# Kernel tuning notes

Measured on AMD Instinct MI355X. Metric: run time of the kernel, lower is better.

## Reference

```python
import jax, jax.numpy as jnp
import numpy as np

B, T, H, M = 64, 1024, 512, 256  # batch, max_time, out_dim(=annot_dim), memory_dim


def setup_inputs() -> dict:
    key = jax.random.key(0)
    ks = jax.random.split(key, 13)
    s = lambda k, shape, scale=1.0: jax.random.normal(k, shape, dtype=jnp.float32) * scale
    return {
        "memory": s(ks[0], (B, M)),
        "context": s(ks[1], (B, H)),
        "rnn_state": s(ks[2], (B, H)),
        "annotations": s(ks[3], (B, T, H)),
        "W_ih": s(ks[4], (3 * H, H + M), 0.04),
        "b_ih": s(ks[5], (3 * H,), 0.04),
        "W_hh": s(ks[6], (3 * H, H), 0.04),
        "b_hh": s(ks[7], (3 * H,), 0.04),
        "Wq": s(ks[8], (H, H), 0.04),
        "bq": s(ks[9], (H,), 0.04),
        "Wa": s(ks[10], (H, H), 0.04),
        "ba": s(ks[11], (H,), 0.04),
        "v": s(ks[12], (H,), 0.04),
    }


def reference(memory, context, rnn_state, annotations,
              W_ih, b_ih, W_hh, b_hh, Wq, bq, Wa, ba, v):
    # --- GRUCell step (torch semantics) ---
    x = jnp.concatenate([memory, context], axis=-1)          # (B, M+H)
    gi = x @ W_ih.T + b_ih                                   # (B, 3H)
    gh = rnn_state @ W_hh.T + b_hh                           # (B, 3H)
    i_r, i_z, i_n = jnp.split(gi, 3, axis=-1)
    h_r, h_z, h_n = jnp.split(gh, 3, axis=-1)
    r = jax.nn.sigmoid(i_r + h_r)
    z = jax.nn.sigmoid(i_z + h_z)
    n = jnp.tanh(i_n + r * h_n)
    h_new = (1.0 - z) * n + z * rnn_state                    # (B, H)

    # --- Bahdanau additive attention ---
    pq = h_new @ Wq.T + bq                                   # (B, H)
    pa = annotations @ Wa.T + ba                             # (B, T, H)
    scores = jnp.tanh(pq[:, None, :] + pa) @ v               # (B, T)
    align = jax.nn.softmax(scores, axis=-1)                  # (B, T)
    ctx = jnp.einsum('bt,btd->bd', align, annotations)       # (B, H)
    return (h_new, ctx, align)
```

## Files before the change

### kernel.cpp

```cpp
#include <hip/hip_runtime.h>
#include <hip/hip_bf16.h>


typedef __attribute__((ext_vector_type(8))) __bf16 bf16x8;
typedef __attribute__((ext_vector_type(8))) unsigned short u16x8;
typedef __attribute__((ext_vector_type(4))) float f32x4;

__device__ __forceinline__ unsigned short f2bf(float f) {
    __hip_bfloat16 h = __float2bfloat16(f);
    return __builtin_bit_cast(unsigned short, h);
}
__device__ __forceinline__ float tanh_fast(float x) {
    float e = __expf(2.0f * x);
    return 1.0f - 2.0f / (e + 1.0f);
}
__device__ __forceinline__ float sigmoid_f(float x) {
    return 1.0f / (1.0f + __expf(-x));
}
__device__ __forceinline__ int swz(int x) { return x ^ (((x >> 8) & 7) << 4); }

__global__ __launch_bounds__(256) void wconv_kernel(
    const float* __restrict__ W_ih, const float* __restrict__ W_hh,
    const float* __restrict__ Wq, const float* __restrict__ Wa,
    unsigned short* __restrict__ WihB, unsigned short* __restrict__ WhhB,
    unsigned short* __restrict__ WqB, unsigned short* __restrict__ WaB)
{
    const int cb = blockIdx.x * 4 + (threadIdx.x >> 6);
    const int l = threadIdx.x & 63;
    const float* src;
    unsigned short* dst;
    int K, local, NB, kt;
    if (cb < 2304) {
        src = W_ih; dst = WihB; K = 768; local = cb;
        NB = local / 24; kt = local % 24;
    } else if (cb < 3840) {
        src = W_hh; dst = WhhB; K = 512; local = cb - 2304;
        NB = local >> 4; kt = local & 15;
    } else if (cb < 4352) {
        src = Wq; dst = WqB; K = 512; local = cb - 3840;
        NB = local >> 4; kt = local & 15;
    } else {
        src = Wa; dst = WaB; K = 512; local = cb - 4352;
        NB = local >> 4; kt = local & 15;
    }
    const float* s = src + (size_t)(NB * 16 + (l & 15)) * K + kt * 32 + (l >> 4) * 8;
    float4 f0 = *(const float4*)s;
    float4 f1 = *(const float4*)(s + 4);
    u16x8 p;
    p[0] = f2bf(f0.x); p[1] = f2bf(f0.y); p[2] = f2bf(f0.z); p[3] = f2bf(f0.w);
    p[4] = f2bf(f1.x); p[5] = f2bf(f1.y); p[6] = f2bf(f1.z); p[7] = f2bf(f1.w);
    *(u16x8*)&dst[(size_t)local * 512 + l * 8] = p;
}

#define CVT8(f0, f1, AF)                                                           \
    {                                                                              \
        u16x8 p_;                                                                  \
        p_[0] = f2bf((f0).x); p_[1] = f2bf((f0).y); p_[2] = f2bf((f0).z); p_[3] = f2bf((f0).w); \
        p_[4] = f2bf((f1).x); p_[5] = f2bf((f1).y); p_[6] = f2bf((f1).z); p_[7] = f2bf((f1).w); \
        AF = __builtin_bit_cast(bf16x8, p_);                                       \
    }

__global__ __launch_bounds__(64) void gru_kernel(
    const float* __restrict__ memory, const float* __restrict__ context,
    const float* __restrict__ rnn_state,
    const unsigned short* __restrict__ WihB, const float* __restrict__ b_ih,
    const unsigned short* __restrict__ WhhB, const float* __restrict__ b_hh,
    float* __restrict__ h_new)
{
    const int l = threadIdx.x;
    const int mt = blockIdx.x >> 5;
    const int hb = blockIdx.x & 31;
    const int r = l & 15, g = l >> 4;
    const int row = mt * 16 + r;

    f32x4 a_ir = {0,0,0,0}, a_iz = {0,0,0,0}, a_in = {0,0,0,0};
    f32x4 a_hr = {0,0,0,0}, a_hz = {0,0,0,0}, a_hn = {0,0,0,0};

#pragma unroll
    for (int kt = 0; kt < 8; ++kt) {
        const float* s = memory + (size_t)row * 256 + kt * 32 + g * 8;
        float4 f0 = *(const float4*)s, f1 = *(const float4*)(s + 4);
        bf16x8 af; CVT8(f0, f1, af);
        bf16x8 b0 = __builtin_bit_cast(bf16x8, *(const u16x8*)&WihB[((size_t)(hb) * 24 + kt) * 512 + l * 8]);
        bf16x8 b1 = __builtin_bit_cast(bf16x8, *(const u16x8*)&WihB[((size_t)(32 + hb) * 24 + kt) * 512 + l * 8]);
        bf16x8 b2 = __builtin_bit_cast(bf16x8, *(const u16x8*)&WihB[((size_t)(64 + hb) * 24 + kt) * 512 + l * 8]);
        a_ir = __builtin_amdgcn_mfma_f32_16x16x32_bf16(af, b0, a_ir, 0, 0, 0);
        a_iz = __builtin_amdgcn_mfma_f32_16x16x32_bf16(af, b1, a_iz, 0, 0, 0);
        a_in = __builtin_amdgcn_mfma_f32_16x16x32_bf16(af, b2, a_in, 0, 0, 0);
    }
#pragma unroll
    for (int kt = 8; kt < 24; ++kt) {
        const float* s = context + (size_t)row * 512 + (kt - 8) * 32 + g * 8;
        float4 f0 = *(const float4*)s, f1 = *(const float4*)(s + 4);
        bf16x8 af; CVT8(f0, f1, af);
        bf16x8 b0 = __builtin_bit_cast(bf16x8, *(const u16x8*)&WihB[((size_t)(hb) * 24 + kt) * 512 + l * 8]);
        bf16x8 b1 = __builtin_bit_cast(bf16x8, *(const u16x8*)&WihB[((size_t)(32 + hb) * 24 + kt) * 512 + l * 8]);
        bf16x8 b2 = __builtin_bit_cast(bf16x8, *(const u16x8*)&WihB[((size_t)(64 + hb) * 24 + kt) * 512 + l * 8]);
        a_ir = __builtin_amdgcn_mfma_f32_16x16x32_bf16(af, b0, a_ir, 0, 0, 0);
        a_iz = __builtin_amdgcn_mfma_f32_16x16x32_bf16(af, b1, a_iz, 0, 0, 0);
        a_in = __builtin_amdgcn_mfma_f32_16x16x32_bf16(af, b2, a_in, 0, 0, 0);
    }
#pragma unroll
    for (int kt = 0; kt < 16; ++kt) {
        const float* s = rnn_state + (size_t)row * 512 + kt * 32 + g * 8;
        float4 f0 = *(const float4*)s, f1 = *(const float4*)(s + 4);
        bf16x8 af; CVT8(f0, f1, af);
        bf16x8 b0 = __builtin_bit_cast(bf16x8, *(const u16x8*)&WhhB[((size_t)(hb) * 16 + kt) * 512 + l * 8]);
        bf16x8 b1 = __builtin_bit_cast(bf16x8, *(const u16x8*)&WhhB[((size_t)(32 + hb) * 16 + kt) * 512 + l * 8]);
        bf16x8 b2 = __builtin_bit_cast(bf16x8, *(const u16x8*)&WhhB[((size_t)(64 + hb) * 16 + kt) * 512 + l * 8]);
        a_hr = __builtin_amdgcn_mfma_f32_16x16x32_bf16(af, b0, a_hr, 0, 0, 0);
        a_hz = __builtin_amdgcn_mfma_f32_16x16x32_bf16(af, b1, a_hz, 0, 0, 0);
        a_hn = __builtin_amdgcn_mfma_f32_16x16x32_bf16(af, b2, a_hn, 0, 0, 0);
    }
    const int c = hb * 16 + r;
    const float bir = b_ih[c], biz = b_ih[512 + c], bin = b_ih[1024 + c];
    const float bhr = b_hh[c], bhz = b_hh[512 + c], bhn = b_hh[1024 + c];
#pragma unroll
    for (int r2 = 0; r2 < 4; ++r2) {
        const int m = mt * 16 + g * 4 + r2;
        float rr = sigmoid_f(a_ir[r2] + bir + a_hr[r2] + bhr);
        float zz = sigmoid_f(a_iz[r2] + biz + a_hz[r2] + bhz);
        float nn = tanh_fast(a_in[r2] + bin + rr * (a_hn[r2] + bhn));
        float h0 = rnn_state[(size_t)m * 512 + c];
        h_new[(size_t)m * 512 + c] = (1.f - zz) * nn + zz * h0;
    }
}

__global__ __launch_bounds__(64) void pq_kernel(
    const float* __restrict__ h_new, const unsigned short* __restrict__ WqB,
    const float* __restrict__ bq, const float* __restrict__ ba,
    float* __restrict__ q)
{
    const int l = threadIdx.x;
    const int mt = blockIdx.x >> 5;
    const int hb = blockIdx.x & 31;
    const int r = l & 15, g = l >> 4;
    const int row = mt * 16 + r;
    f32x4 acc = {0,0,0,0};
#pragma unroll
    for (int kt = 0; kt < 16; ++kt) {
        const float* s = h_new + (size_t)row * 512 + kt * 32 + g * 8;
        float4 f0 = *(const float4*)s, f1 = *(const float4*)(s + 4);
        bf16x8 af; CVT8(f0, f1, af);
        bf16x8 b0 = __builtin_bit_cast(bf16x8, *(const u16x8*)&WqB[((size_t)hb * 16 + kt) * 512 + l * 8]);
        acc = __builtin_amdgcn_mfma_f32_16x16x32_bf16(af, b0, acc, 0, 0, 0);
    }
    const int c = hb * 16 + r;
    const float add = bq[c] + ba[c];
#pragma unroll
    for (int r2 = 0; r2 < 4; ++r2)
        q[(size_t)(mt * 16 + g * 4 + r2) * 512 + c] = acc[r2] + add;
}

__global__ __launch_bounds__(256, 2) void scores_kernel(
    const float* __restrict__ ann, const unsigned short* __restrict__ WaB,
    const float* __restrict__ qv, const float* __restrict__ v,
    float* __restrict__ scores)
{
    __shared__ unsigned short As[32768];
    __shared__ float s_sc[64];
    const int tid = threadIdx.x;
    const int l = tid & 63;
    const int w = tid >> 6;
    const int r0 = blockIdx.x * 64;
    const int b = blockIdx.x >> 4;

    if (tid < 64) s_sc[tid] = 0.f;

#pragma unroll
    for (int p = 0; p < 16; ++p) {
        int cidx = tid + p * 256;
        int row = cidx >> 6;
        int c8 = cidx & 63;
        int kt = c8 >> 2, g = c8 & 3;
        int rt = row >> 4, r15 = row & 15;
        const float* s = ann + (size_t)(r0 + row) * 512 + c8 * 8;
        float4 f0 = *(const float4*)s, f1 = *(const float4*)(s + 4);
        u16x8 pk;
        pk[0] = f2bf(f0.x); pk[1] = f2bf(f0.y); pk[2] = f2bf(f0.z); pk[3] = f2bf(f0.w);
        pk[4] = f2bf(f1.x); pk[5] = f2bf(f1.y); pk[6] = f2bf(f1.z); pk[7] = f2bf(f1.w);
        int logical = (((rt * 16 + kt) * 64) + g * 16 + r15) * 16;
        *(u16x8*)((char*)As + swz(logical)) = pk;
    }
    __syncthreads();

    f32x4 acc[4][8];
#pragma unroll
    for (int i = 0; i < 4; ++i)
#pragma unroll
        for (int j = 0; j < 8; ++j) acc[i][j] = (f32x4){0.f, 0.f, 0.f, 0.f};

#pragma unroll 2
    for (int kt = 0; kt < 16; ++kt) {
        u16x8 bv[8];
#pragma unroll
        for (int ct = 0; ct < 8; ++ct)
            bv[ct] = *(const u16x8*)(WaB + ((size_t)((w * 8 + ct) * 16 + kt)) * 512 + l * 8);
#pragma unroll
        for (int rt = 0; rt < 4; ++rt) {
            int logical = ((rt * 16 + kt) * 64 + l) * 16;
            bf16x8 af = __builtin_bit_cast(bf16x8, *(const u16x8*)((char*)As + swz(logical)));
#pragma unroll
            for (int ct = 0; ct < 8; ++ct)
                acc[rt][ct] = __builtin_amdgcn_mfma_f32_16x16x32_bf16(
                    af, __builtin_bit_cast(bf16x8, bv[ct]), acc[rt][ct], 0, 0, 0);
        }
    }

    float rsum[4][4];
#pragma unroll
    for (int i = 0; i < 4; ++i)
#pragma unroll
        for (int j = 0; j < 4; ++j) rsum[i][j] = 0.f;

#pragma unroll
    for (int ct = 0; ct < 8; ++ct) {
        int col = w * 128 + ct * 16 + (l & 15);
        float qq = qv[b * 512 + col];
        float vv = v[col];
#pragma unroll
        for (int rt = 0; rt < 4; ++rt) {
            f32x4 a = acc[rt][ct];
#pragma unroll
            for (int r2 = 0; r2 < 4; ++r2)
                rsum[rt][r2] += tanh_fast(a[r2] + qq) * vv;
        }
    }
#pragma unroll
    for (int m = 1; m < 16; m <<= 1) {
#pragma unroll
        for (int rt = 0; rt < 4; ++rt)
#pragma unroll
            for (int r2 = 0; r2 < 4; ++r2)
                rsum[rt][r2] += __shfl_xor(rsum[rt][r2], m, 64);
    }
    if ((l & 15) == 0) {
        int g = l >> 4;
#pragma unroll
        for (int rt = 0; rt < 4; ++rt)
#pragma unroll
            for (int r2 = 0; r2 < 4; ++r2)
                atomicAdd(&s_sc[rt * 16 + g * 4 + r2], rsum[rt][r2]);
    }
    __syncthreads();
    if (tid < 64) scores[r0 + tid] = s_sc[tid];
}

__global__ __launch_bounds__(256) void softmax_kernel(
    const float* __restrict__ scores, float* __restrict__ align_)
{
    const int b = blockIdx.x, tid = threadIdx.x;
    __shared__ float red[256];
    float s[4];
#pragma unroll
    for (int j = 0; j < 4; ++j) s[j] = scores[b * 1024 + j * 256 + tid];
    float mx = fmaxf(fmaxf(s[0], s[1]), fmaxf(s[2], s[3]));
    red[tid] = mx; __syncthreads();
    for (int off = 128; off > 0; off >>= 1) {
        if (tid < off) red[tid] = fmaxf(red[tid], red[tid + off]);
        __syncthreads();
    }
    mx = red[0]; __syncthreads();
    float e[4], sum = 0.f;
#pragma unroll
    for (int j = 0; j < 4; ++j) { e[j] = __expf(s[j] - mx); sum += e[j]; }
    red[tid] = sum; __syncthreads();
    for (int off = 128; off > 0; off >>= 1) {
        if (tid < off) red[tid] += red[tid + off];
        __syncthreads();
    }
    float inv = 1.0f / red[0];
#pragma unroll
    for (int j = 0; j < 4; ++j) align_[b * 1024 + j * 256 + tid] = e[j] * inv;
}

__global__ __launch_bounds__(256) void ctx_part_kernel(
    const float* __restrict__ ann, const float* __restrict__ align_,
    float* __restrict__ part)
{
    const int tid = threadIdx.x;
    const int b = blockIdx.x;
    const int tc = blockIdx.y;
    __shared__ float al[128];
    __shared__ float4 red[128];
    if (tid < 128) al[tid] = align_[b * 1024 + tc * 128 + tid];
    __syncthreads();
    const int rp = tid >> 7, d4 = (tid & 127) * 4;
    const float* ap = ann + ((size_t)(b * 1024 + tc * 128)) * 512 + d4;
    float4 acc = {0.f, 0.f, 0.f, 0.f};
    for (int tt = rp; tt < 128; tt += 2) {
        float4 x = *(const float4*)(ap + (size_t)tt * 512);
        float wv = al[tt];
        acc.x += wv * x.x; acc.y += wv * x.y; acc.z += wv * x.z; acc.w += wv * x.w;
    }
    if (rp == 1) red[tid & 127] = acc;
    __syncthreads();
    if (rp == 0) {
        float4 o = red[tid];
        o.x += acc.x; o.y += acc.y; o.z += acc.z; o.w += acc.w;
        *(float4*)&part[((size_t)(tc * 64 + b)) * 512 + d4] = o;
    }
}

__global__ __launch_bounds__(256) void ctx_reduce_kernel(
    const float* __restrict__ part, float* __restrict__ ctx)
{
    int i4 = (blockIdx.x * 256 + threadIdx.x) * 4;
    float4 s = {0.f, 0.f, 0.f, 0.f};
#pragma unroll
    for (int p = 0; p < 8; ++p) {
        float4 x = *(const float4*)&part[(size_t)p * 32768 + i4];
        s.x += x.x; s.y += x.y; s.z += x.z; s.w += x.w;
    }
    *(float4*)&ctx[i4] = s;
}

extern "C" void kernel_launch(void* const* d_in, const int* in_sizes, int n_in,
                              void* d_out, int out_size, void* d_ws, size_t ws_size,
                              hipStream_t stream)
{
    (void)in_sizes; (void)n_in; (void)out_size; (void)ws_size;
    const float* memory    = (const float*)d_in[0];
    const float* context   = (const float*)d_in[1];
    const float* rnn_state = (const float*)d_in[2];
    const float* ann       = (const float*)d_in[3];
    const float* W_ih      = (const float*)d_in[4];
    const float* b_ih      = (const float*)d_in[5];
    const float* W_hh      = (const float*)d_in[6];
    const float* b_hh      = (const float*)d_in[7];
    const float* Wq        = (const float*)d_in[8];
    const float* bq        = (const float*)d_in[9];
    const float* Wa        = (const float*)d_in[10];
    const float* ba        = (const float*)d_in[11];
    const float* v         = (const float*)d_in[12];

    float* out    = (float*)d_out;
    float* h_new  = out;
    float* ctx    = out + 32768;
    float* align_ = out + 65536;

    char* wsb = (char*)d_ws;
    float* q    = (float*)(wsb + 0);
    float* sc   = (float*)(wsb + 131072);
    float* part = (float*)(wsb + 393216);
    unsigned short* WihB = (unsigned short*)(wsb + 1441792);
    unsigned short* WhhB = (unsigned short*)(wsb + 3801088);
    unsigned short* WqB  = (unsigned short*)(wsb + 5373952);
    unsigned short* WaB  = (unsigned short*)(wsb + 5898240);

    wconv_kernel<<<dim3(1216), dim3(256), 0, stream>>>(
        W_ih, W_hh, Wq, Wa, WihB, WhhB, WqB, WaB);
    gru_kernel<<<dim3(128), dim3(64), 0, stream>>>(
        memory, context, rnn_state, WihB, b_ih, WhhB, b_hh, h_new);
    pq_kernel<<<dim3(128), dim3(64), 0, stream>>>(h_new, WqB, bq, ba, q);
    scores_kernel<<<dim3(1024), dim3(256), 0, stream>>>(ann, WaB, q, v, sc);
    softmax_kernel<<<dim3(64), dim3(256), 0, stream>>>(sc, align_);
    ctx_part_kernel<<<dim3(64, 8), dim3(256), 0, stream>>>(ann, align_, part);
    ctx_reduce_kernel<<<dim3(32), dim3(256), 0, stream>>>(part, ctx);
}
```

Measured before the change: 110.0 us.

## Double scores tile to 128 rows with 8 waves and double-buffered B loads

The scores kernel now processes 128 annotation rows per block with 512 threads arranged as 2x4 waves, so each loaded Wa fragment is reused across twice as many rows per block. The annotation loads become nontemporal, and the K loop prefetches the next Wa fragment set while MFMAs run on the current one. This trades higher LDS use (128KB per block) and register pressure for fewer blocks and less Wa refetch traffic. With launch bounds of 512x2 and 128KB LDS, occupancy may effectively be limited to one block per CU.

```diff
diff --git a/kernel.cpp b/kernel.cpp
--- a/kernel.cpp
+++ b/kernel.cpp
@@ -5,6 +5,7 @@
 typedef __attribute__((ext_vector_type(8))) __bf16 bf16x8;
 typedef __attribute__((ext_vector_type(8))) unsigned short u16x8;
 typedef __attribute__((ext_vector_type(4))) float f32x4;
+typedef __attribute__((ext_vector_type(4))) float f4v;
 
 __device__ __forceinline__ unsigned short f2bf(float f) {
     __hip_bfloat16 h = __float2bfloat16(f);
@@ -18,6 +19,9 @@
     return 1.0f / (1.0f + __expf(-x));
 }
 __device__ __forceinline__ int swz(int x) { return x ^ (((x >> 8) & 7) << 4); }
+__device__ __forceinline__ f4v ntload4(const float* p) {
+    return __builtin_nontemporal_load((const f4v*)p);
+}
 
 __global__ __launch_bounds__(256) void wconv_kernel(
     const float* __restrict__ W_ih, const float* __restrict__ W_hh,
@@ -152,34 +156,37 @@
         q[(size_t)(mt * 16 + g * 4 + r2) * 512 + c] = acc[r2] + add;
 }
 
-__global__ __launch_bounds__(256, 2) void scores_kernel(
+__global__ __launch_bounds__(512, 2) void scores_kernel(
     const float* __restrict__ ann, const unsigned short* __restrict__ WaB,
     const float* __restrict__ qv, const float* __restrict__ v,
     float* __restrict__ scores)
 {
-    __shared__ unsigned short As[32768];
-    __shared__ float s_sc[64];
+    __shared__ unsigned short As[65536];
+    __shared__ float s_sc[128];
     const int tid = threadIdx.x;
     const int l = tid & 63;
     const int w = tid >> 6;
-    const int r0 = blockIdx.x * 64;
-    const int b = blockIdx.x >> 4;
-
-    if (tid < 64) s_sc[tid] = 0.f;
+    const int wr = w >> 2;
+    const int wc = w & 3;
+    const int r0 = blockIdx.x * 128;
+    const int b = blockIdx.x >> 3;
+
+    if (tid < 128) s_sc[tid] = 0.f;
 
 #pragma unroll
     for (int p = 0; p < 16; ++p) {
-        int cidx = tid + p * 256;
+        int cidx = tid + p * 512;
         int row = cidx >> 6;
         int c8 = cidx & 63;
         int kt = c8 >> 2, g = c8 & 3;
-        int rt = row >> 4, r15 = row & 15;
+        int rtg = row >> 4, r15 = row & 15;
         const float* s = ann + (size_t)(r0 + row) * 512 + c8 * 8;
-        float4 f0 = *(const float4*)s, f1 = *(const float4*)(s + 4);
+        f4v f0 = ntload4(s);
+        f4v f1 = ntload4(s + 4);
         u16x8 pk;
-        pk[0] = f2bf(f0.x); pk[1] = f2bf(f0.y); pk[2] = f2bf(f0.z); pk[3] = f2bf(f0.w);
-        pk[4] = f2bf(f1.x); pk[5] = f2bf(f1.y); pk[6] = f2bf(f1.z); pk[7] = f2bf(f1.w);
-        int logical = (((rt * 16 + kt) * 64) + g * 16 + r15) * 16;
+        pk[0] = f2bf(f0[0]); pk[1] = f2bf(f0[1]); pk[2] = f2bf(f0[2]); pk[3] = f2bf(f0[3]);
+        pk[4] = f2bf(f1[0]); pk[5] = f2bf(f1[1]); pk[6] = f2bf(f1[2]); pk[7] = f2bf(f1[3]);
+        int logical = (((rtg * 16 + kt) * 64) + g * 16 + r15) * 16;
         *(u16x8*)((char*)As + swz(logical)) = pk;
     }
     __syncthreads();
@@ -190,22 +197,38 @@
 #pragma unroll
         for (int j = 0; j < 8; ++j) acc[i][j] = (f32x4){0.f, 0.f, 0.f, 0.f};
 
-#pragma unroll 2
-    for (int kt = 0; kt < 16; ++kt) {
-        u16x8 bv[8];
-#pragma unroll
-        for (int ct = 0; ct < 8; ++ct)
-            bv[ct] = *(const u16x8*)(WaB + ((size_t)((w * 8 + ct) * 16 + kt)) * 512 + l * 8);
-#pragma unroll
-        for (int rt = 0; rt < 4; ++rt) {
-            int logical = ((rt * 16 + kt) * 64 + l) * 16;
-            bf16x8 af = __builtin_bit_cast(bf16x8, *(const u16x8*)((char*)As + swz(logical)));
-#pragma unroll
-            for (int ct = 0; ct < 8; ++ct)
-                acc[rt][ct] = __builtin_amdgcn_mfma_f32_16x16x32_bf16(
-                    af, __builtin_bit_cast(bf16x8, bv[ct]), acc[rt][ct], 0, 0, 0);
-        }
-    }
+#define LOADB(BV, ktv)                                                                 \
+    {                                                                                  \
+        _Pragma("unroll")                                                              \
+        for (int ct_ = 0; ct_ < 8; ++ct_)                                              \
+            BV[ct_] = *(const u16x8*)(WaB +                                            \
+                ((size_t)((wc * 8 + ct_) * 16 + (ktv))) * 512 + l * 8);                \
+    }
+
+#define MFMA_K(ktv, BV)                                                                \
+    {                                                                                  \
+        _Pragma("unroll")                                                              \
+        for (int rt_ = 0; rt_ < 4; ++rt_) {                                            \
+            int logical = (((wr * 4 + rt_) * 16 + (ktv)) * 64 + l) * 16;               \
+            bf16x8 af_ = __builtin_bit_cast(bf16x8,                                    \
+                *(const u16x8*)((char*)As + swz(logical)));                            \
+            _Pragma("unroll")                                                          \
+            for (int ct_ = 0; ct_ < 8; ++ct_)                                          \
+                acc[rt_][ct_] = __builtin_amdgcn_mfma_f32_16x16x32_bf16(               \
+                    af_, __builtin_bit_cast(bf16x8, BV[ct_]), acc[rt_][ct_], 0, 0, 0); \
+        }                                                                              \
+    }
+
+    u16x8 bvE[8], bvO[8];
+    LOADB(bvE, 0);
+    for (int kt2 = 0; kt2 < 8; ++kt2) {
+        LOADB(bvO, 2 * kt2 + 1);
+        MFMA_K(2 * kt2, bvE);
+        if (kt2 < 7) LOADB(bvE, 2 * kt2 + 2);
+        MFMA_K(2 * kt2 + 1, bvO);
+    }
+#undef LOADB
+#undef MFMA_K
 
     float rsum[4][4];
 #pragma unroll
@@ -215,7 +238,7 @@
 
 #pragma unroll
     for (int ct = 0; ct < 8; ++ct) {
-        int col = w * 128 + ct * 16 + (l & 15);
+        int col = wc * 128 + ct * 16 + (l & 15);
         float qq = qv[b * 512 + col];
         float vv = v[col];
 #pragma unroll
@@ -240,10 +263,10 @@
         for (int rt = 0; rt < 4; ++rt)
 #pragma unroll
             for (int r2 = 0; r2 < 4; ++r2)
-                atomicAdd(&s_sc[rt * 16 + g * 4 + r2], rsum[rt][r2]);
+                atomicAdd(&s_sc[wr * 64 + rt * 16 + g * 4 + r2], rsum[rt][r2]);
     }
     __syncthreads();
-    if (tid < 64) scores[r0 + tid] = s_sc[tid];
+    if (tid < 128) scores[r0 + tid] = s_sc[tid];
 }
 
 __global__ __launch_bounds__(256) void softmax_kernel(
@@ -353,7 +376,7 @@
     gru_kernel<<<dim3(128), dim3(64), 0, stream>>>(
         memory, context, rnn_state, WihB, b_ih, WhhB, b_hh, h_new);
     pq_kernel<<<dim3(128), dim3(64), 0, stream>>>(h_new, WqB, bq, ba, q);
-    scores_kernel<<<dim3(1024), dim3(256), 0, stream>>>(ann, WaB, q, v, sc);
+    scores_kernel<<<dim3(512), dim3(512), 0, stream>>>(ann, WaB, q, v, sc);
     softmax_kernel<<<dim3(64), dim3(256), 0, stream>>>(sc, align_);
     ctx_part_kernel<<<dim3(64, 8), dim3(256), 0, stream>>>(ann, align_, part);
     ctx_reduce_kernel<<<dim3(32), dim3(256), 0, stream>>>(part, ctx);
```

Measured after the change: 130.2 us. 1.18x slower.
